# Kernel optimization log

Measured on AMD Instinct MI355X. Metric: run time of the kernel, lower is better.

The kernel has to match this reference:

```python
import jax, jax.numpy as jnp
import numpy as np

N_SPACE = 197  # spatial tokens (ViT-B/16: 196 patches + CLS)
T = 8          # frames, fixed by space_time_pos shape (197*8, dim)
H = 12         # heads


def setup_inputs() -> dict:
    key = jax.random.key(0)
    ks = jax.random.split(key, 8)
    dim = 768
    B = 8
    Nq = 1576
    scale = dim ** -0.5
    return {
        "s_x": jax.random.normal(ks[0], (N_SPACE, B * T, dim), jnp.float32),
        "t_x": jax.random.normal(ks[1], (B, Nq, dim), jnp.float32),
        "space_time_pos": scale * jax.random.normal(ks[2], (N_SPACE * T, dim), jnp.float32),
        "q_w": jax.random.normal(ks[3], (dim, dim), jnp.float32) * 0.02,
        "q_b": jnp.zeros((dim,), jnp.float32),
        "kv_w": jax.random.normal(ks[4], (2 * dim, dim), jnp.float32) * 0.02,
        "kv_b": jnp.zeros((2 * dim,), jnp.float32),
        "proj_w": jax.random.normal(ks[5], (dim, dim), jnp.float32) * 0.02,
        "proj_b": jnp.zeros((dim,), jnp.float32),
    }


def reference(s_x, t_x, space_time_pos, q_w, q_b, kv_w, kv_b, proj_w, proj_b):
    n, BT, dim = s_x.shape
    B, Nq, _ = t_x.shape
    t = BT // B
    head_dim = dim // H
    scale = head_dim ** -0.5

    # rearrange 'n (b t) d -> b (t n) d'
    s = s_x.reshape(n, B, t, dim).transpose(1, 2, 0, 3).reshape(B, t * n, dim)
    s = s + space_time_pos  # (B, t*n, dim)

    # Q from t_x, K/V from s
    q = t_x @ q_w.T + q_b                      # (B, Nq, dim)
    kv = s @ kv_w.T + kv_b                     # (B, t*n, 2*dim)
    Nk = t * n
    # 'b n (e h d) -> e b h n d'
    kv = kv.reshape(B, Nk, 2, H, head_dim).transpose(2, 0, 3, 1, 4)
    k, v = kv[0], kv[1]                        # (B, H, Nk, hd)
    q = q.reshape(B, Nq, H, head_dim).transpose(0, 2, 1, 3) * scale  # (B, H, Nq, hd)

    attn = jnp.einsum('bhqd,bhkd->bhqk', q, k)
    attn = jax.nn.softmax(attn, axis=-1)
    out = jnp.einsum('bhqk,bhkd->bhqd', attn, v)   # (B, H, Nq, hd)
    out = out.transpose(0, 2, 1, 3).reshape(B, Nq, dim)
    return out @ proj_w.T + proj_b
```

## Files before the change

### kernel.cpp

```cpp
#include <hip/hip_runtime.h>
#include <stdint.h>

#define NSPACE 197
#define TFRAMES 8
#define NH 12
#define DIM 768
#define HD 64
#define BATCH 8
#define NQ 1576
#define NK 1576
#define M_REAL 12608
#define M_PAD 12672
#define VT_LD 1600

typedef __attribute__((ext_vector_type(8))) short s16x8;
typedef __attribute__((ext_vector_type(4))) short s16x4;
typedef __attribute__((ext_vector_type(4))) float f32x4;

__device__ inline uint16_t f2bf(float f) {
    union { float f; uint32_t i; } c; c.f = f;
    uint32_t r = c.i + 0x7FFF + ((c.i >> 16) & 1);
    return (uint16_t)(r >> 16);
}

__device__ inline uint32_t cvtpk_bf16(float lo, float hi) {
    uint32_t r;
    asm("v_cvt_pk_bf16_f32 %0, %1, %2" : "=v"(r) : "v"(lo), "v"(hi));
    return r;
}

__device__ inline float exp2_raw(float x) { return __builtin_amdgcn_exp2f(x); }

__device__ inline void gld_lds16(const uint16_t* g, uint16_t* l) {
    __builtin_amdgcn_global_load_lds(
        (const __attribute__((address_space(1))) void*)g,
        (__attribute__((address_space(3))) void*)l,
        16, 0, 0);
}

#define FILLB 4752
#define CONVQ_B 288
#define CONVKV_B 576
__global__ void prep(const float* __restrict__ t_x, const float* __restrict__ s_x,
                     const float* __restrict__ pos,
                     const float* __restrict__ q_w, const float* __restrict__ kv_w,
                     uint16_t* __restrict__ x_pad, uint16_t* __restrict__ s_pad,
                     uint16_t* __restrict__ wq, uint16_t* __restrict__ wkv) {
    int bx = blockIdx.x, tid = threadIdx.x;
    if (bx < FILLB) {
        int chunk = bx * 256 + tid;
        size_t off = (size_t)chunk * 8;
        s16x8 o;
        if (off < (size_t)M_REAL * DIM) {
            float4 a = *(const float4*)(t_x + off);
            float4 b = *(const float4*)(t_x + off + 4);
            union { s16x8 v; uint32_t u[4]; } p;
            p.u[0] = cvtpk_bf16(a.x, a.y);
            p.u[1] = cvtpk_bf16(a.z, a.w);
            p.u[2] = cvtpk_bf16(b.x, b.y);
            p.u[3] = cvtpk_bf16(b.z, b.w);
            o = p.v;
        } else {
            for (int j = 0; j < 8; j++) o[j] = 0;
        }
        *(s16x8*)(x_pad + off) = o;
    } else if (bx < 2 * FILLB) {
        int chunk = (bx - FILLB) * 256 + tid;
        int i = chunk / (DIM / 8);
        int cc = chunk - i * (DIM / 8);
        int d0 = cc * 8;
        uint16_t* dst = s_pad + (size_t)i * DIM + d0;
        if (i >= M_REAL) {
            s16x8 z; for (int j = 0; j < 8; j++) z[j] = 0;
            *(s16x8*)dst = z;
            return;
        }
        int b = i / NK, rr = i - b * NK;
        int t_i = rr / NSPACE, n_i = rr - t_i * NSPACE;
        const float* src = s_x + ((size_t)(n_i * (BATCH * TFRAMES) + b * TFRAMES + t_i)) * DIM + d0;
        const float* ps = pos + (size_t)rr * DIM + d0;
        float4 a0 = *(const float4*)src;
        float4 a1 = *(const float4*)(src + 4);
        float4 p0 = *(const float4*)ps;
        float4 p1 = *(const float4*)(ps + 4);
        union { s16x8 v; uint32_t u[4]; } o;
        o.u[0] = cvtpk_bf16(a0.x + p0.x, a0.y + p0.y);
        o.u[1] = cvtpk_bf16(a0.z + p0.z, a0.w + p0.w);
        o.u[2] = cvtpk_bf16(a1.x + p1.x, a1.y + p1.y);
        o.u[3] = cvtpk_bf16(a1.z + p1.z, a1.w + p1.w);
        *(s16x8*)dst = o.v;
    } else if (bx < 2 * FILLB + CONVQ_B) {
        int chunk = (bx - 2 * FILLB) * 256 + tid;
        size_t off = (size_t)chunk * 8;
        float4 a = *(const float4*)(q_w + off);
        float4 b = *(const float4*)(q_w + off + 4);
        union { s16x8 v; uint32_t u[4]; } o;
        o.u[0] = cvtpk_bf16(a.x, a.y);
        o.u[1] = cvtpk_bf16(a.z, a.w);
        o.u[2] = cvtpk_bf16(b.x, b.y);
        o.u[3] = cvtpk_bf16(b.z, b.w);
        *(s16x8*)(wq + off) = o.v;
    } else {
        int chunk = (bx - 2 * FILLB - CONVQ_B) * 256 + tid;
        size_t off = (size_t)chunk * 8;
        float4 a = *(const float4*)(kv_w + off);
        float4 b = *(const float4*)(kv_w + off + 4);
        union { s16x8 v; uint32_t u[4]; } o;
        o.u[0] = cvtpk_bf16(a.x, a.y);
        o.u[1] = cvtpk_bf16(a.z, a.w);
        o.u[2] = cvtpk_bf16(b.x, b.y);
        o.u[3] = cvtpk_bf16(b.z, b.w);
        *(s16x8*)(wkv + off) = o.v;
    }
}

__global__ void conv_f2b(const float* __restrict__ src, uint16_t* __restrict__ dst, int n8) {
    int chunk = blockIdx.x * 256 + threadIdx.x;
    if (chunk >= n8) return;
    size_t off = (size_t)chunk * 8;
    float4 a = *(const float4*)(src + off);
    float4 b = *(const float4*)(src + off + 4);
    union { s16x8 v; uint32_t u[4]; } o;
    o.u[0] = cvtpk_bf16(a.x, a.y);
    o.u[1] = cvtpk_bf16(a.z, a.w);
    o.u[2] = cvtpk_bf16(b.x, b.y);
    o.u[3] = cvtpk_bf16(b.z, b.w);
    *(s16x8*)(dst + off) = o.v;
}

template <int MODE>
__global__ __launch_bounds__(256)
void gemm_bt(const uint16_t* __restrict__ A, const uint16_t* __restrict__ W,
             const float* __restrict__ bias,
             uint16_t* __restrict__ out0, uint16_t* __restrict__ out1,
             float* __restrict__ outf) {
    __shared__ uint16_t As[128 * 32];
    __shared__ uint16_t Bs[128 * 32];
    const int t = threadIdx.x;
    const int lane = t & 63, w = t >> 6;
    const int r16 = lane & 15, quad = lane >> 4;
    const int wm = w >> 1, wn = w & 1;
    const int m0 = blockIdx.y * 128;
    const int n0 = blockIdx.x * 128;

    const int srow = w * 32 + (lane >> 2);
    const int scol = (lane & 3) * 8;
    const uint16_t* Ag = A + (size_t)(m0 + srow) * DIM + scol;
    const uint16_t* Wg = W + (size_t)(n0 + srow) * DIM + scol;
    uint16_t* Asw = &As[w * 32 * 32];
    uint16_t* Bsw = &Bs[w * 32 * 32];

    f32x4 acc[4][4];
    for (int a = 0; a < 4; a++)
        for (int bb = 0; bb < 4; bb++)
            for (int r = 0; r < 4; r++) acc[a][bb][r] = 0.f;

    for (int kk = 0; kk < DIM; kk += 32) {
        gld_lds16(Ag + kk, Asw);
        gld_lds16(Ag + kk + (size_t)16 * DIM, Asw + 16 * 32);
        gld_lds16(Wg + kk, Bsw);
        gld_lds16(Wg + kk + (size_t)16 * DIM, Bsw + 16 * 32);
        __syncthreads();
        s16x8 af[4], bfr[4];
        for (int mt = 0; mt < 4; mt++)
            af[mt] = *(const s16x8*)&As[(wm * 64 + mt * 16 + r16) * 32 + quad * 8];
        for (int nt = 0; nt < 4; nt++)
            bfr[nt] = *(const s16x8*)&Bs[(wn * 64 + nt * 16 + r16) * 32 + quad * 8];
        for (int mt = 0; mt < 4; mt++)
            for (int nt = 0; nt < 4; nt++)
                acc[mt][nt] = __builtin_amdgcn_mfma_f32_16x16x32_bf16(af[mt], bfr[nt], acc[mt][nt], 0, 0, 0);
        __syncthreads();
    }

    for (int mt = 0; mt < 4; mt++)
        for (int nt = 0; nt < 4; nt++) {
            int col = n0 + wn * 64 + nt * 16 + r16;
            float bz = bias[col];
            int rowb = m0 + wm * 64 + mt * 16 + quad * 4;
            for (int r = 0; r < 4; r++) {
                int i = rowb + r;
                if (i >= M_REAL) continue;
                float v = acc[mt][nt][r] + bz;
                if (MODE == 0) {
                    int b = i / NQ, nq = i - b * NQ;
                    int h = col >> 6, d = col & 63;
                    out0[(size_t)(((b * NH + h) * NQ) + nq) * HD + d] = f2bf(v * 0.18033688011112042f);
                } else if (MODE == 1) {
                    int b = i / NK, nk = i - b * NK;
                    if (col < DIM) {
                        int h = col >> 6, d = col & 63;
                        out0[(size_t)(((b * NH + h) * NK) + nk) * HD + d] = f2bf(v);
                    } else {
                        int c2 = col - DIM;
                        int h = c2 >> 6, d = c2 & 63;
                        out1[(size_t)(((b * NH + h) * NK) + nk) * HD + d] = f2bf(v);
                    }
                } else {
                    outf[(size_t)i * DIM + col] = v;
                }
            }
        }
}

__global__ __launch_bounds__(256)
void transpose_v(const uint16_t* __restrict__ v, uint16_t* __restrict__ vt) {
    __shared__ uint16_t T[64 * 72];
    int tile = blockIdx.x, bh = blockIdx.y;
    int nk0 = tile * 64;
    const uint16_t* V = v + (size_t)bh * NK * HD;
    uint16_t* VT = vt + (size_t)bh * HD * VT_LD;
    int tid = threadIdx.x;
    int rr = tid >> 3;
    int c8 = (tid & 7) * 8;
    for (int p = 0; p < 2; p++) {
        int lr = p * 32 + rr;
        int nk = nk0 + lr;
        s16x8 val;
        if (nk < NK) val = *(const s16x8*)(V + (size_t)nk * HD + c8);
        else for (int j = 0; j < 8; j++) val[j] = 0;
        for (int j = 0; j < 8; j++)
            T[(c8 + j) * 72 + lr] = (uint16_t)val[j];
    }
    __syncthreads();
    for (int p = 0; p < 2; p++) {
        int d = p * 32 + rr;
        s16x8 o = *(const s16x8*)&T[d * 72 + c8];
        *(s16x8*)(VT + (size_t)d * VT_LD + nk0 + c8) = o;
    }
}

#define NITER 50
__global__ __launch_bounds__(256)
void flash_attn(const uint16_t* __restrict__ q_buf, const uint16_t* __restrict__ k_buf,
                const uint16_t* __restrict__ vt_buf, uint16_t* __restrict__ ao) {
    __shared__ uint16_t Kb[2][32 * 72];
    __shared__ uint16_t Vb[2][64 * 40];
    int h = blockIdx.y, b = blockIdx.z;
    int tid = threadIdx.x;
    int lane = tid & 63, w = tid >> 6;
    int r16 = lane & 15, quad = lane >> 4;
    size_t bh = (size_t)(b * NH + h);
    const uint16_t* Q = q_buf + bh * NQ * HD;
    const uint16_t* K = k_buf + bh * NK * HD;
    const uint16_t* VT = vt_buf + bh * HD * VT_LD;
    int q0 = blockIdx.x * 128 + w * 32;

    const int kg = tid >> 3;
    const int kc = (tid & 7) * 8;
    const int kslot = ((kg >> 3) << 2) + (kg & 3) + ((kg & 4) ? 16 : 0);
    const int vd = tid >> 2;
    const int vc = (tid & 3) * 8;
    const uint16_t* Kg = K + (size_t)kg * HD + kc;
    const uint16_t* Vg = VT + (size_t)vd * VT_LD + vc;
    uint16_t* Kw = &Kb[0][kslot * 72 + kc];
    uint16_t* Vw = &Vb[0][vd * 40 + vc];
    const int KBSZ = 32 * 72, VBSZ = 64 * 40;

    s16x8 qf[2][2];
    for (int m = 0; m < 2; m++) {
        int qrow = q0 + m * 16 + r16;
        if (qrow < NQ) {
            qf[m][0] = *(const s16x8*)(Q + (size_t)qrow * HD + quad * 8);
            qf[m][1] = *(const s16x8*)(Q + (size_t)qrow * HD + 32 + quad * 8);
        } else {
            for (int j = 0; j < 8; j++) { qf[m][0][j] = 0; qf[m][1][j] = 0; }
        }
    }

    f32x4 z4;
    for (int r = 0; r < 4; r++) z4[r] = 0.f;
    s16x8 ones;
    for (int j = 0; j < 8; j++) ones[j] = (short)0x3F80;

    f32x4 oT[2][4];
    f32x4 oLs[2];
    for (int m = 0; m < 2; m++) {
        for (int dt = 0; dt < 4; dt++)
            for (int r = 0; r < 4; r++) oT[m][dt][r] = 0.f;
        for (int r = 0; r < 4; r++) oLs[m][r] = 0.f;
    }

    {
        s16x8 kv = *(const s16x8*)Kg;
        s16x8 vv = *(const s16x8*)Vg;
        *(s16x8*)Kw = kv;
        *(s16x8*)Vw = vv;
    }
    __syncthreads();

    for (int it = 0; it < NITER - 1; it++) {
        int kb = it * 32;
        int cur = it & 1, nxt = cur ^ 1;
        s16x8 knv = *(const s16x8*)(Kg + (size_t)(kb + 32) * HD);
        s16x8 vnv = *(const s16x8*)(Vg + kb + 32);

        const uint16_t* Kc = &Kb[cur][0];
        const uint16_t* Vc = &Vb[cur][0];
        s16x8 kfA0 = *(const s16x8*)(Kc + r16 * 72 + quad * 8);
        s16x8 kfA1 = *(const s16x8*)(Kc + r16 * 72 + 32 + quad * 8);
        s16x8 kfB0 = *(const s16x8*)(Kc + (16 + r16) * 72 + quad * 8);
        s16x8 kfB1 = *(const s16x8*)(Kc + (16 + r16) * 72 + 32 + quad * 8);

        s16x8 pf[2];
        #pragma unroll
        for (int m = 0; m < 2; m++) {
            f32x4 sA = __builtin_amdgcn_mfma_f32_16x16x32_bf16(kfA0, qf[m][0], z4, 0, 0, 0);
            sA = __builtin_amdgcn_mfma_f32_16x16x32_bf16(kfA1, qf[m][1], sA, 0, 0, 0);
            f32x4 sB = __builtin_amdgcn_mfma_f32_16x16x32_bf16(kfB0, qf[m][0], z4, 0, 0, 0);
            sB = __builtin_amdgcn_mfma_f32_16x16x32_bf16(kfB1, qf[m][1], sB, 0, 0, 0);
            f32x4 pA, pB;
            #pragma unroll
            for (int r = 0; r < 4; r++) { pA[r] = exp2_raw(sA[r]); pB[r] = exp2_raw(sB[r]); }
            union { s16x8 v; uint32_t u[4]; } pk;
            pk.u[0] = cvtpk_bf16(pA[0], pA[1]);
            pk.u[1] = cvtpk_bf16(pA[2], pA[3]);
            pk.u[2] = cvtpk_bf16(pB[0], pB[1]);
            pk.u[3] = cvtpk_bf16(pB[2], pB[3]);
            pf[m] = pk.v;
        }
        #pragma unroll
        for (int dt = 0; dt < 4; dt++) {
            s16x8 vf = *(const s16x8*)(Vc + (dt * 16 + r16) * 40 + quad * 8);
            oT[0][dt] = __builtin_amdgcn_mfma_f32_16x16x32_bf16(vf, pf[0], oT[0][dt], 0, 0, 0);
            oT[1][dt] = __builtin_amdgcn_mfma_f32_16x16x32_bf16(vf, pf[1], oT[1][dt], 0, 0, 0);
        }
        oLs[0] = __builtin_amdgcn_mfma_f32_16x16x32_bf16(ones, pf[0], oLs[0], 0, 0, 0);
        oLs[1] = __builtin_amdgcn_mfma_f32_16x16x32_bf16(ones, pf[1], oLs[1], 0, 0, 0);
        *(s16x8*)(Kw + nxt * KBSZ) = knv;
        *(s16x8*)(Vw + nxt * VBSZ) = vnv;
        __syncthreads();
    }

    {
        const int it = NITER - 1;
        const int kb = it * 32;
        const int cur = it & 1;
        const uint16_t* Kc = &Kb[cur][0];
        const uint16_t* Vc = &Vb[cur][0];
        s16x8 kfA0 = *(const s16x8*)(Kc + r16 * 72 + quad * 8);
        s16x8 kfA1 = *(const s16x8*)(Kc + r16 * 72 + 32 + quad * 8);
        s16x8 kfB0 = *(const s16x8*)(Kc + (16 + r16) * 72 + quad * 8);
        s16x8 kfB1 = *(const s16x8*)(Kc + (16 + r16) * 72 + 32 + quad * 8);

        s16x8 pf[2];
        #pragma unroll
        for (int m = 0; m < 2; m++) {
            f32x4 sA = __builtin_amdgcn_mfma_f32_16x16x32_bf16(kfA0, qf[m][0], z4, 0, 0, 0);
            sA = __builtin_amdgcn_mfma_f32_16x16x32_bf16(kfA1, qf[m][1], sA, 0, 0, 0);
            f32x4 sB = __builtin_amdgcn_mfma_f32_16x16x32_bf16(kfB0, qf[m][0], z4, 0, 0, 0);
            sB = __builtin_amdgcn_mfma_f32_16x16x32_bf16(kfB1, qf[m][1], sB, 0, 0, 0);
            f32x4 pA, pB;
            #pragma unroll
            for (int r = 0; r < 4; r++) {
                pA[r] = (kb + quad * 8 + r < NK)     ? exp2_raw(sA[r]) : 0.f;
                pB[r] = (kb + quad * 8 + 4 + r < NK) ? exp2_raw(sB[r]) : 0.f;
            }
            union { s16x8 v; uint32_t u[4]; } pk;
            pk.u[0] = cvtpk_bf16(pA[0], pA[1]);
            pk.u[1] = cvtpk_bf16(pA[2], pA[3]);
            pk.u[2] = cvtpk_bf16(pB[0], pB[1]);
            pk.u[3] = cvtpk_bf16(pB[2], pB[3]);
            pf[m] = pk.v;
        }
        #pragma unroll
        for (int dt = 0; dt < 4; dt++) {
            s16x8 vf = *(const s16x8*)(Vc + (dt * 16 + r16) * 40 + quad * 8);
            oT[0][dt] = __builtin_amdgcn_mfma_f32_16x16x32_bf16(vf, pf[0], oT[0][dt], 0, 0, 0);
            oT[1][dt] = __builtin_amdgcn_mfma_f32_16x16x32_bf16(vf, pf[1], oT[1][dt], 0, 0, 0);
        }
        oLs[0] = __builtin_amdgcn_mfma_f32_16x16x32_bf16(ones, pf[0], oLs[0], 0, 0, 0);
        oLs[1] = __builtin_amdgcn_mfma_f32_16x16x32_bf16(ones, pf[1], oLs[1], 0, 0, 0);
    }

    #pragma unroll
    for (int m = 0; m < 2; m++) {
        float rs = oLs[m][0];
        int q = q0 + m * 16 + r16;
        if (q >= NQ) continue;
        float inv = 1.0f / rs;
        size_t rowoff = (size_t)(b * NQ + q) * DIM + h * HD;
        #pragma unroll
        for (int dt = 0; dt < 4; dt++) {
            union { s16x4 v; uint32_t u[2]; } o;
            o.u[0] = cvtpk_bf16(oT[m][dt][0] * inv, oT[m][dt][1] * inv);
            o.u[1] = cvtpk_bf16(oT[m][dt][2] * inv, oT[m][dt][3] * inv);
            *(s16x4*)(ao + rowoff + dt * 16 + quad * 4) = o.v;
        }
    }
}

extern "C" void kernel_launch(void* const* d_in, const int* in_sizes, int n_in,
                              void* d_out, int out_size, void* d_ws, size_t ws_size,
                              hipStream_t stream) {
    const float* s_x    = (const float*)d_in[0];
    const float* t_x    = (const float*)d_in[1];
    const float* pos    = (const float*)d_in[2];
    const float* q_w    = (const float*)d_in[3];
    const float* q_b    = (const float*)d_in[4];
    const float* kv_w   = (const float*)d_in[5];
    const float* kv_b   = (const float*)d_in[6];
    const float* proj_w = (const float*)d_in[7];
    const float* proj_b = (const float*)d_in[8];
    float* out = (float*)d_out;

    char* ws = (char*)d_ws;
    size_t off = 0;
    auto carve = [&](size_t bytes) {
        void* p = ws + off;
        off += (bytes + 255) & ~(size_t)255;
        return p;
    };
    uint16_t* x_pad   = (uint16_t*)carve((size_t)M_PAD * DIM * 2);
    uint16_t* s_pad   = (uint16_t*)carve((size_t)M_PAD * DIM * 2);
    uint16_t* q_buf   = (uint16_t*)carve((size_t)BATCH * NH * NQ * HD * 2);
    uint16_t* k_buf   = (uint16_t*)carve((size_t)BATCH * NH * NK * HD * 2);
    uint16_t* vt_buf  = (uint16_t*)carve((size_t)BATCH * NH * HD * VT_LD * 2);
    uint16_t* wq_buf  = (uint16_t*)carve((size_t)DIM * DIM * 2);
    uint16_t* wkv_buf = (uint16_t*)carve((size_t)2 * DIM * DIM * 2);
    if (off > ws_size) return;
    uint16_t* v_buf = x_pad;
    uint16_t* ao    = x_pad;
    uint16_t* wproj = wq_buf;

    const int wq8 = DIM * DIM / 8;
    const int prep_blocks = 2 * FILLB + CONVQ_B + CONVKV_B;

    prep<<<prep_blocks, 256, 0, stream>>>(t_x, s_x, pos, q_w, kv_w,
                                          x_pad, s_pad, wq_buf, wkv_buf);

    gemm_bt<0><<<dim3(DIM / 128, M_PAD / 128), 256, 0, stream>>>(x_pad, wq_buf, q_b, q_buf, nullptr, nullptr);
    gemm_bt<1><<<dim3(2 * DIM / 128, M_PAD / 128), 256, 0, stream>>>(s_pad, wkv_buf, kv_b, k_buf, v_buf, nullptr);
    transpose_v<<<dim3(VT_LD / 64, BATCH * NH), 256, 0, stream>>>(v_buf, vt_buf);

    conv_f2b<<<(wq8 + 255) / 256, 256, 0, stream>>>(proj_w, wproj, wq8);

    flash_attn<<<dim3((NQ + 127) / 128, NH, BATCH), 256, 0, stream>>>(q_buf, k_buf, vt_buf, ao);

    gemm_bt<2><<<dim3(DIM / 128, M_PAD / 128), 256, 0, stream>>>(ao, wproj, proj_b, nullptr, nullptr, out);
}
```

Before: 360.9 us.

## Halve per-wave query tile, remap grid for XCD locality, sum softmax denominators in VALU

The flash attention kernel now gives each wave 16 query rows instead of 32, so a workgroup covers 64 queries and the grid grows to 2400 blocks. It uses a flat 1D grid with an XCD-aware remap so consecutive work items for the same head land on the same chiplet. The row-sum MFMA with a ones vector is replaced by VALU accumulation of the probabilities plus cross-lane shuffles at the end. This trades more parallelism and occupancy for twice the K/V shared-memory loads per query, with less reuse of each K/V tile.

New measurement: 369.2 us. +2.3%, slower.

```diff
diff --git a/kernel.cpp b/kernel.cpp
--- a/kernel.cpp
+++ b/kernel.cpp
@@ -230,12 +230,19 @@
 }
 
 #define NITER 50
+#define NQB 25
+#define FLASH_WG 2400
 __global__ __launch_bounds__(256)
 void flash_attn(const uint16_t* __restrict__ q_buf, const uint16_t* __restrict__ k_buf,
                 const uint16_t* __restrict__ vt_buf, uint16_t* __restrict__ ao) {
     __shared__ uint16_t Kb[2][32 * 72];
     __shared__ uint16_t Vb[2][64 * 40];
-    int h = blockIdx.y, b = blockIdx.z;
+    int wgid = blockIdx.x;
+    int work = (wgid & 7) * (FLASH_WG / 8) + (wgid >> 3);
+    int qb = work % NQB;
+    int hb = work / NQB;
+    int h = hb % NH;
+    int b = hb / NH;
     int tid = threadIdx.x;
     int lane = tid & 63, w = tid >> 6;
     int r16 = lane & 15, quad = lane >> 4;
@@ -243,7 +250,7 @@
     const uint16_t* Q = q_buf + bh * NQ * HD;
     const uint16_t* K = k_buf + bh * NK * HD;
     const uint16_t* VT = vt_buf + bh * HD * VT_LD;
-    int q0 = blockIdx.x * 128 + w * 32;
+    int q0 = qb * 64 + w * 16;
 
     const int kg = tid >> 3;
     const int kc = (tid & 7) * 8;
@@ -256,29 +263,25 @@
     uint16_t* Vw = &Vb[0][vd * 40 + vc];
     const int KBSZ = 32 * 72, VBSZ = 64 * 40;
 
-    s16x8 qf[2][2];
-    for (int m = 0; m < 2; m++) {
-        int qrow = q0 + m * 16 + r16;
+    s16x8 qf[2];
+    {
+        int qrow = q0 + r16;
         if (qrow < NQ) {
-            qf[m][0] = *(const s16x8*)(Q + (size_t)qrow * HD + quad * 8);
-            qf[m][1] = *(const s16x8*)(Q + (size_t)qrow * HD + 32 + quad * 8);
+            qf[0] = *(const s16x8*)(Q + (size_t)qrow * HD + quad * 8);
+            qf[1] = *(const s16x8*)(Q + (size_t)qrow * HD + 32 + quad * 8);
         } else {
-            for (int j = 0; j < 8; j++) { qf[m][0][j] = 0; qf[m][1][j] = 0; }
+            for (int j = 0; j < 8; j++) { qf[0][j] = 0; qf[1][j] = 0; }
         }
     }
 
     f32x4 z4;
     for (int r = 0; r < 4; r++) z4[r] = 0.f;
-    s16x8 ones;
-    for (int j = 0; j < 8; j++) ones[j] = (short)0x3F80;
-
-    f32x4 oT[2][4];
-    f32x4 oLs[2];
-    for (int m = 0; m < 2; m++) {
-        for (int dt = 0; dt < 4; dt++)
-            for (int r = 0; r < 4; r++) oT[m][dt][r] = 0.f;
-        for (int r = 0; r < 4; r++) oLs[m][r] = 0.f;
-    }
+
+    f32x4 oT[4];
+    f32x4 lsum4;
+    for (int dt = 0; dt < 4; dt++)
+        for (int r = 0; r < 4; r++) oT[dt][r] = 0.f;
+    for (int r = 0; r < 4; r++) lsum4[r] = 0.f;
 
     {
         s16x8 kv = *(const s16x8*)Kg;
@@ -301,31 +304,27 @@
         s16x8 kfB0 = *(const s16x8*)(Kc + (16 + r16) * 72 + quad * 8);
         s16x8 kfB1 = *(const s16x8*)(Kc + (16 + r16) * 72 + 32 + quad * 8);
 
-        s16x8 pf[2];
+        f32x4 sA = __builtin_amdgcn_mfma_f32_16x16x32_bf16(kfA0, qf[0], z4, 0, 0, 0);
+        sA = __builtin_amdgcn_mfma_f32_16x16x32_bf16(kfA1, qf[1], sA, 0, 0, 0);
+        f32x4 sB = __builtin_amdgcn_mfma_f32_16x16x32_bf16(kfB0, qf[0], z4, 0, 0, 0);
+        sB = __builtin_amdgcn_mfma_f32_16x16x32_bf16(kfB1, qf[1], sB, 0, 0, 0);
+        f32x4 pA, pB;
         #pragma unroll
-        for (int m = 0; m < 2; m++) {
-            f32x4 sA = __builtin_amdgcn_mfma_f32_16x16x32_bf16(kfA0, qf[m][0], z4, 0, 0, 0);
-            sA = __builtin_amdgcn_mfma_f32_16x16x32_bf16(kfA1, qf[m][1], sA, 0, 0, 0);
-            f32x4 sB = __builtin_amdgcn_mfma_f32_16x16x32_bf16(kfB0, qf[m][0], z4, 0, 0, 0);
-            sB = __builtin_amdgcn_mfma_f32_16x16x32_bf16(kfB1, qf[m][1], sB, 0, 0, 0);
-            f32x4 pA, pB;
-            #pragma unroll
-            for (int r = 0; r < 4; r++) { pA[r] = exp2_raw(sA[r]); pB[r] = exp2_raw(sB[r]); }
-            union { s16x8 v; uint32_t u[4]; } pk;
-            pk.u[0] = cvtpk_bf16(pA[0], pA[1]);
-            pk.u[1] = cvtpk_bf16(pA[2], pA[3]);
-            pk.u[2] = cvtpk_bf16(pB[0], pB[1]);
-            pk.u[3] = cvtpk_bf16(pB[2], pB[3]);
-            pf[m] = pk.v;
-        }
+        for (int r = 0; r < 4; r++) { pA[r] = exp2_raw(sA[r]); pB[r] = exp2_raw(sB[r]); }
+        lsum4 += pA;
+        lsum4 += pB;
+        union { s16x8 v; uint32_t u[4]; } pk;
+        pk.u[0] = cvtpk_bf16(pA[0], pA[1]);
+        pk.u[1] = cvtpk_bf16(pA[2], pA[3]);
+        pk.u[2] = cvtpk_bf16(pB[0], pB[1]);
+        pk.u[3] = cvtpk_bf16(pB[2], pB[3]);
+        s16x8 pf = pk.v;
+
         #pragma unroll
         for (int dt = 0; dt < 4; dt++) {
             s16x8 vf = *(const s16x8*)(Vc + (dt * 16 + r16) * 40 + quad * 8);
-            oT[0][dt] = __builtin_amdgcn_mfma_f32_16x16x32_bf16(vf, pf[0], oT[0][dt], 0, 0, 0);
-            oT[1][dt] = __builtin_amdgcn_mfma_f32_16x16x32_bf16(vf, pf[1], oT[1][dt], 0, 0, 0);
-        }
-        oLs[0] = __builtin_amdgcn_mfma_f32_16x16x32_bf16(ones, pf[0], oLs[0], 0, 0, 0);
-        oLs[1] = __builtin_amdgcn_mfma_f32_16x16x32_bf16(ones, pf[1], oLs[1], 0, 0, 0);
+            oT[dt] = __builtin_amdgcn_mfma_f32_16x16x32_bf16(vf, pf, oT[dt], 0, 0, 0);
+        }
         *(s16x8*)(Kw + nxt * KBSZ) = knv;
         *(s16x8*)(Vw + nxt * VBSZ) = vnv;
         __syncthreads();
@@ -342,49 +341,47 @@
         s16x8 kfB0 = *(const s16x8*)(Kc + (16 + r16) * 72 + quad * 8);
         s16x8 kfB1 = *(const s16x8*)(Kc + (16 + r16) * 72 + 32 + quad * 8);
 
-        s16x8 pf[2];
+        f32x4 sA = __builtin_amdgcn_mfma_f32_16x16x32_bf16(kfA0, qf[0], z4, 0, 0, 0);
+        sA = __builtin_amdgcn_mfma_f32_16x16x32_bf16(kfA1, qf[1], sA, 0, 0, 0);
+        f32x4 sB = __builtin_amdgcn_mfma_f32_16x16x32_bf16(kfB0, qf[0], z4, 0, 0, 0);
+        sB = __builtin_amdgcn_mfma_f32_16x16x32_bf16(kfB1, qf[1], sB, 0, 0, 0);
+        f32x4 pA, pB;
         #pragma unroll
-        for (int m = 0; m < 2; m++) {
-            f32x4 sA = __builtin_amdgcn_mfma_f32_16x16x32_bf16(kfA0, qf[m][0], z4, 0, 0, 0);
-            sA = __builtin_amdgcn_mfma_f32_16x16x32_bf16(kfA1, qf[m][1], sA, 0, 0, 0);
-            f32x4 sB = __builtin_amdgcn_mfma_f32_16x16x32_bf16(kfB0, qf[m][0], z4, 0, 0, 0);
-            sB = __builtin_amdgcn_mfma_f32_16x16x32_bf16(kfB1, qf[m][1], sB, 0, 0, 0);
-            f32x4 pA, pB;
-            #pragma unroll
-            for (int r = 0; r < 4; r++) {
-                pA[r] = (kb + quad * 8 + r < NK)     ? exp2_raw(sA[r]) : 0.f;
-                pB[r] = (kb + quad * 8 + 4 + r < NK) ? exp2_raw(sB[r]) : 0.f;
-            }
-            union { s16x8 v; uint32_t u[4]; } pk;
-            pk.u[0] = cvtpk_bf16(pA[0], pA[1]);
-            pk.u[1] = cvtpk_bf16(pA[2], pA[3]);
-            pk.u[2] = cvtpk_bf16(pB[0], pB[1]);
-            pk.u[3] = cvtpk_bf16(pB[2], pB[3]);
-            pf[m] = pk.v;
-        }
+        for (int r = 0; r < 4; r++) {
+            pA[r] = (kb + quad * 8 + r < NK)     ? exp2_raw(sA[r]) : 0.f;
+            pB[r] = (kb + quad * 8 + 4 + r < NK) ? exp2_raw(sB[r]) : 0.f;
+        }
+        lsum4 += pA;
+        lsum4 += pB;
+        union { s16x8 v; uint32_t u[4]; } pk;
+        pk.u[0] = cvtpk_bf16(pA[0], pA[1]);
+        pk.u[1] = cvtpk_bf16(pA[2], pA[3]);
+        pk.u[2] = cvtpk_bf16(pB[0], pB[1]);
+        pk.u[3] = cvtpk_bf16(pB[2], pB[3]);
+        s16x8 pf = pk.v;
+
         #pragma unroll
         for (int dt = 0; dt < 4; dt++) {
             s16x8 vf = *(const s16x8*)(Vc + (dt * 16 + r16) * 40 + quad * 8);
-            oT[0][dt] = __builtin_amdgcn_mfma_f32_16x16x32_bf16(vf, pf[0], oT[0][dt], 0, 0, 0);
-            oT[1][dt] = __builtin_amdgcn_mfma_f32_16x16x32_bf16(vf, pf[1], oT[1][dt], 0, 0, 0);
-        }
-        oLs[0] = __builtin_amdgcn_mfma_f32_16x16x32_bf16(ones, pf[0], oLs[0], 0, 0, 0);
-        oLs[1] = __builtin_amdgcn_mfma_f32_16x16x32_bf16(ones, pf[1], oLs[1], 0, 0, 0);
-    }
-
-    #pragma unroll
-    for (int m = 0; m < 2; m++) {
-        float rs = oLs[m][0];
-        int q = q0 + m * 16 + r16;
-        if (q >= NQ) continue;
-        float inv = 1.0f / rs;
-        size_t rowoff = (size_t)(b * NQ + q) * DIM + h * HD;
-        #pragma unroll
-        for (int dt = 0; dt < 4; dt++) {
-            union { s16x4 v; uint32_t u[2]; } o;
-            o.u[0] = cvtpk_bf16(oT[m][dt][0] * inv, oT[m][dt][1] * inv);
-            o.u[1] = cvtpk_bf16(oT[m][dt][2] * inv, oT[m][dt][3] * inv);
-            *(s16x4*)(ao + rowoff + dt * 16 + quad * 4) = o.v;
+            oT[dt] = __builtin_amdgcn_mfma_f32_16x16x32_bf16(vf, pf, oT[dt], 0, 0, 0);
+        }
+    }
+
+    {
+        float rs = lsum4[0] + lsum4[1] + lsum4[2] + lsum4[3];
+        rs += __shfl_xor(rs, 16);
+        rs += __shfl_xor(rs, 32);
+        int q = q0 + r16;
+        if (q < NQ) {
+            float inv = 1.0f / rs;
+            size_t rowoff = (size_t)(b * NQ + q) * DIM + h * HD;
+            #pragma unroll
+            for (int dt = 0; dt < 4; dt++) {
+                union { s16x4 v; uint32_t u[2]; } o;
+                o.u[0] = cvtpk_bf16(oT[dt][0] * inv, oT[dt][1] * inv);
+                o.u[1] = cvtpk_bf16(oT[dt][2] * inv, oT[dt][3] * inv);
+                *(s16x4*)(ao + rowoff + dt * 16 + quad * 4) = o.v;
+            }
         }
     }
 }
@@ -434,7 +431,7 @@
 
     conv_f2b<<<(wq8 + 255) / 256, 256, 0, stream>>>(proj_w, wproj, wq8);
 
-    flash_attn<<<dim3((NQ + 127) / 128, NH, BATCH), 256, 0, stream>>>(q_buf, k_buf, vt_buf, ao);
+    flash_attn<<<FLASH_WG, 256, 0, stream>>>(q_buf, k_buf, vt_buf, ao);
 
     gemm_bt<2><<<dim3(DIM / 128, M_PAD / 128), 256, 0, stream>>>(ao, wproj, proj_b, nullptr, nullptr, out);
 }
```
